# Performance work log

Hardware: AMD Instinct MI355X
Metric: run time of the kernel (lower is better)

## Reference

```python
import jax, jax.numpy as jnp
import numpy as np

NUM_HEADS = 16
DIM_HEADS = 64
DIM_INPUT = 1024
DIM = NUM_HEADS * DIM_HEADS  # 1024


def setup_inputs() -> dict:
    key = jax.random.key(0)
    ks = jax.random.split(key, 8)
    B, S = 2, 2048
    inputs = jax.random.normal(ks[0], (B, S, DIM_INPUT), dtype=jnp.float32)
    attention_mask = jnp.zeros((B, 1, 1, S), dtype=jnp.float32)
    s = 1.0 / np.sqrt(DIM_INPUT)
    Wq = jax.random.normal(ks[1], (DIM_INPUT, DIM), dtype=jnp.float32) * s
    bq = jnp.zeros((DIM,), dtype=jnp.float32)
    Wk = jax.random.normal(ks[2], (DIM_INPUT, DIM), dtype=jnp.float32) * s
    bk = jnp.zeros((DIM,), dtype=jnp.float32)
    Wv = jax.random.normal(ks[3], (DIM_INPUT, DIM), dtype=jnp.float32) * s
    bv = jnp.zeros((DIM,), dtype=jnp.float32)
    return {"inputs": inputs, "attention_mask": attention_mask,
            "Wq": Wq, "bq": bq, "Wk": Wk, "bk": bk, "Wv": Wv, "bv": bv}


def _split_heads(x):
    # [B, S, H*dh] -> [B, H, S, dh]
    B, S, _ = x.shape
    return x.reshape(B, S, NUM_HEADS, DIM_HEADS).transpose(0, 2, 1, 3)


def reference(inputs, attention_mask, Wq, bq, Wk, bk, Wv, bv):
    q = _split_heads(inputs @ Wq + bq)  # [B,H,S,dh]
    k = _split_heads(inputs @ Wk + bk)
    v = _split_heads(inputs @ Wv + bv)
    scores = jnp.einsum('bhsd,bhtd->bhst', q, k) / np.sqrt(DIM_HEADS).astype(np.float32)
    scores = scores + attention_mask  # broadcast additive mask
    probs = jax.nn.softmax(scores, axis=-1)  # dropout is identity in eval
    ctx = jnp.einsum('bhst,bhtd->bhsd', probs, v)  # [B,H,S,dh]
    B, H, S, dh = ctx.shape
    return ctx.transpose(0, 2, 1, 3).reshape(B, S, H * dh)
```

## Files before the change

### kernel.cpp

```cpp
#include <hip/hip_runtime.h>


typedef __attribute__((ext_vector_type(4))) float f32x4;
typedef __attribute__((ext_vector_type(16))) float f32x16;
typedef __attribute__((ext_vector_type(8))) __bf16 bf16x8;

#define DEV static __device__ __forceinline__

constexpr int S_ = 2048;
constexpr int H_ = 16;
constexpr int DH_ = 64;
constexpr int DIN_ = 1024;
constexpr int M_ = 2 * S_;
constexpr int N3_ = 3 * 1024;
constexpr int K_ = DIN_;
constexpr float LOG2E = 1.44269504088896340736f;

DEV unsigned short f2bf(float f) {
  unsigned u = __builtin_bit_cast(unsigned, f);
  u += 0x7fffu + ((u >> 16) & 1u);
  return (unsigned short)(u >> 16);
}

DEV unsigned cvt_pk(float lo, float hi) {
  unsigned d;
  asm("v_cvt_pk_bf16_f32 %0, %1, %2" : "=v"(d) : "v"(lo), "v"(hi));
  return d;
}

DEV void gload_lds16(const void* g, void* l) {
  __builtin_amdgcn_global_load_lds(
      (const __attribute__((address_space(1))) unsigned int*)g,
      (__attribute__((address_space(3))) unsigned int*)l, 16, 0, 0);
}

DEV int kswz(int row, int colb) { return row * 128 + (colb ^ ((row & 7) << 4)); }

__global__ __launch_bounds__(256) void convert_x(const float* __restrict__ X,
                                                 unsigned short* __restrict__ Xbf) {
  int idx = (blockIdx.x * 256 + threadIdx.x) * 8;
  float4 a = *(const float4*)(X + idx);
  float4 b = *(const float4*)(X + idx + 4);
  unsigned short r[8];
  r[0] = f2bf(a.x); r[1] = f2bf(a.y); r[2] = f2bf(a.z); r[3] = f2bf(a.w);
  r[4] = f2bf(b.x); r[5] = f2bf(b.y); r[6] = f2bf(b.z); r[7] = f2bf(b.w);
  *(uint4*)(Xbf + idx) = *(uint4*)r;
}

__global__ __launch_bounds__(256) void transpose_w(const float* __restrict__ Wq,
                                                   const float* __restrict__ Wk,
                                                   const float* __restrict__ Wv,
                                                   unsigned short* __restrict__ Wt) {
  __shared__ float tile[32][33];
  int z = blockIdx.z;
  const float* W = (z == 0) ? Wq : (z == 1) ? Wk : Wv;
  int n0 = blockIdx.x * 32, k0 = blockIdx.y * 32;
  int tx = threadIdx.x, ty = threadIdx.y;
  for (int i = 0; i < 4; ++i)
    tile[ty + i * 8][tx] = W[(size_t)(k0 + ty + i * 8) * 1024 + n0 + tx];
  __syncthreads();
  for (int i = 0; i < 4; ++i)
    Wt[(size_t)(z * 1024 + n0 + ty + i * 8) * 1024 + k0 + tx] =
        f2bf(tile[tx][ty + i * 8]);
}

__global__ __launch_bounds__(256, 2) void qkv_gemm(
    const unsigned short* __restrict__ Xbf, const unsigned short* __restrict__ Wt,
    const float* __restrict__ bq, const float* __restrict__ bk,
    const float* __restrict__ bv, unsigned short* __restrict__ Qw,
    unsigned short* __restrict__ Kw, unsigned short* __restrict__ Vt) {
  __shared__ unsigned short Abuf[128 * 64];
  __shared__ unsigned short Bbuf[128 * 64];
  int tid = threadIdx.x;
  int w = tid >> 6, l = tid & 63;
  int row16 = l & 15, kg = l >> 4;
  int mBase = blockIdx.y * 128, nBase = blockIdx.x * 128;
  int wm = w >> 1, wn = w & 1;

  f32x4 acc[4][4] = {};

  const int grow = l >> 3;
  const int gcol = ((l & 7) ^ grow) * 8;

  for (int kt = 0; kt < K_ / 64; ++kt) {
    int k0 = kt * 64;
    __syncthreads();
#pragma unroll
    for (int j = 0; j < 4; ++j) {
      int c1k = w * 4 + j;
      int r = c1k * 8 + grow;
      gload_lds16(Xbf + (size_t)(mBase + r) * K_ + k0 + gcol,
                  (char*)Abuf + c1k * 1024);
      gload_lds16(Wt + (size_t)(nBase + r) * K_ + k0 + gcol,
                  (char*)Bbuf + c1k * 1024);
    }
    __syncthreads();
#pragma unroll
    for (int kk = 0; kk < 2; ++kk) {
      bf16x8 af[4], bfr[4];
#pragma unroll
      for (int m = 0; m < 4; ++m)
        af[m] = *(const bf16x8*)((const char*)Abuf +
                 kswz(wm * 64 + m * 16 + row16, kk * 64 + kg * 16));
#pragma unroll
      for (int n = 0; n < 4; ++n)
        bfr[n] = *(const bf16x8*)((const char*)Bbuf +
                  kswz(wn * 64 + n * 16 + row16, kk * 64 + kg * 16));
#pragma unroll
      for (int m = 0; m < 4; ++m)
#pragma unroll
        for (int n = 0; n < 4; ++n)
          acc[m][n] = __builtin_amdgcn_mfma_f32_16x16x32_bf16(af[m], bfr[n],
                                                              acc[m][n], 0, 0, 0);
    }
  }

#pragma unroll
  for (int n = 0; n < 4; ++n) {
    int gn = nBase + wn * 64 + n * 16 + row16;
    int which = gn >> 10;
    int nn = gn & 1023;
    float bias = (which == 0 ? bq : which == 1 ? bk : bv)[nn];
    unsigned short* dst = (which == 0) ? Qw : (which == 1) ? Kw : Vt;
    float scl = (which == 0) ? 0.125f * LOG2E : 1.0f;
    int hh = nn >> 6, dd = nn & 63;
#pragma unroll
    for (int m = 0; m < 4; ++m) {
      int gm0 = mBase + wm * 64 + m * 16 + kg * 4;
#pragma unroll
      for (int j = 0; j < 4; ++j) {
        int gm = gm0 + j;
        int bb = gm >> 11, ss = gm & 2047;
        float v = (acc[m][n][j] + bias) * scl;
        size_t idx;
        if (which == 2) {
          int cs = (ss & ~63) | ((ss & 63) ^ ((dd & 7) << 3));
          idx = ((size_t)(bb * H_ + hh) * DH_ + dd) * S_ + cs;
        } else if (which == 1) {
          idx = ((size_t)(bb * H_ + hh) * S_ + ss) * DH_ + (dd ^ ((ss & 7) << 3));
        } else {
          idx = ((size_t)(bb * H_ + hh) * S_ + ss) * DH_ + dd;
        }
        dst[idx] = f2bf(v);
      }
    }
  }
}

__global__ __launch_bounds__(256, 2) void attn_fwd(
    const unsigned short* __restrict__ Qw, const unsigned short* __restrict__ Kw,
    const unsigned short* __restrict__ Vt, const float* __restrict__ mask,
    float* __restrict__ out) {
  __shared__ __align__(16) char LDS[73728];

  const int tid = threadIdx.x;
  const int w = tid >> 6, l = tid & 63;
  const int qg = w >> 1, thalf = w & 1;
  const int lq = l & 31, h = l >> 5;
  const int wgid = blockIdx.x;
  const int xcd = wgid & 7, ixd = wgid >> 3;
  const int bh = xcd + 8 * (ixd >> 4);
  const int qt = ixd & 15;
  const int b = bh >> 4, hh = bh & 15;
  const int q0 = qt * 128 + qg * 64;

  const char* KbB = (const char*)(Kw + (size_t)bh * S_ * DH_);
  const char* VbB = (const char*)(Vt + (size_t)bh * DH_ * S_);

  {
    const float* mrow = mask + (size_t)b * S_ + tid * 8;
    float4 m0 = *(const float4*)mrow;
    float4 m1 = *(const float4*)(mrow + 4);
    m0.x *= LOG2E; m0.y *= LOG2E; m0.z *= LOG2E; m0.w *= LOG2E;
    m1.x *= LOG2E; m1.y *= LOG2E; m1.z *= LOG2E; m1.w *= LOG2E;
    *(float4*)(LDS + tid * 32) = m0;
    *(float4*)(LDS + tid * 32 + 16) = m1;
  }

  bf16x8 qfA[4], qfB[4];
  {
    const unsigned short* qa = Qw + ((size_t)bh * S_ + q0 + lq) * DH_;
    const unsigned short* qb = qa + 32 * DH_;
#pragma unroll
    for (int kk = 0; kk < 4; ++kk) {
      qfA[kk] = *(const bf16x8*)(qa + kk * 16 + h * 8);
      qfB[kk] = *(const bf16x8*)(qb + kk * 16 + h * 8);
    }
  }

  int rb[4];
#pragma unroll
  for (int kk = 0; kk < 4; ++kk)
    rb[kk] = 8192 + thalf * 8192 + lq * 128 +
             ((kk * 32 + h * 16) ^ ((lq & 7) << 4));

  int voff[4];
#pragma unroll
  for (int i = 0; i < 4; ++i) {
    int Lb = (w * 4 + i) * 1024 + l * 16;
    voff[i] = ((Lb >> 7) & 63) * (S_ * 2) + (Lb >> 13) * 128 + (Lb & 127);
  }

  auto stage = [&](int pair, int buf) __attribute__((always_inline)) {
#pragma unroll
    for (int i = 0; i < 4; ++i) {
      const int c = w * 4 + i;
      gload_lds16(KbB + (size_t)pair * 16384 + c * 1024 + l * 16,
                  LDS + 8192 + buf * 16384 + c * 1024);
      gload_lds16(VbB + (size_t)pair * 256 + voff[i],
                  LDS + 40960 + buf * 16384 + c * 1024);
    }
  };

  stage(0, 0);
  __syncthreads();

  float lA = 0.f, lB = 0.f;
  f32x16 OA0 = {}, OA1 = {}, OB0 = {}, OB1 = {};

  auto body = [&](int p, int cur) __attribute__((always_inline)) {
    if (p < 15) stage(p + 1, cur ^ 1);

    const int mo = thalf * 256 + h * 16 + p * 512;
    f32x16 pA0, pA1, pB0, pB1;
#pragma unroll
    for (int r2 = 0; r2 < 4; ++r2) {
      f32x4 a = *(const f32x4*)(LDS + mo + r2 * 32);
      f32x4 b4 = *(const f32x4*)(LDS + mo + 128 + r2 * 32);
#pragma unroll
      for (int c = 0; c < 4; ++c) {
        pA0[4 * r2 + c] = a[c];  pB0[4 * r2 + c] = a[c];
        pA1[4 * r2 + c] = b4[c]; pB1[4 * r2 + c] = b4[c];
      }
    }

    __builtin_amdgcn_s_setprio(1);
#pragma unroll
    for (int kk = 0; kk < 4; ++kk) {
      bf16x8 kf0 = *(const bf16x8*)(LDS + rb[kk] + cur * 16384);
      bf16x8 kf1 = *(const bf16x8*)(LDS + rb[kk] + 4096 + cur * 16384);
      pA0 = __builtin_amdgcn_mfma_f32_32x32x16_bf16(kf0, qfA[kk], pA0, 0, 0, 0);
      pB0 = __builtin_amdgcn_mfma_f32_32x32x16_bf16(kf0, qfB[kk], pB0, 0, 0, 0);
      pA1 = __builtin_amdgcn_mfma_f32_32x32x16_bf16(kf1, qfA[kk], pA1, 0, 0, 0);
      pB1 = __builtin_amdgcn_mfma_f32_32x32x16_bf16(kf1, qfB[kk], pB1, 0, 0, 0);
    }
    __builtin_amdgcn_s_setprio(0);

#pragma unroll
    for (int i = 0; i < 16; ++i) {
      pA0[i] = __builtin_amdgcn_exp2f(pA0[i]);
      pA1[i] = __builtin_amdgcn_exp2f(pA1[i]);
      pB0[i] = __builtin_amdgcn_exp2f(pB0[i]);
      pB1[i] = __builtin_amdgcn_exp2f(pB1[i]);
    }

    {
      float sA[8], sB[8];
#pragma unroll
      for (int i = 0; i < 8; ++i) {
        sA[i] = (pA0[i] + pA0[i + 8]) + (pA1[i] + pA1[i + 8]);
        sB[i] = (pB0[i] + pB0[i + 8]) + (pB1[i] + pB1[i + 8]);
      }
      float rsA = ((sA[0] + sA[1]) + (sA[2] + sA[3])) +
                  ((sA[4] + sA[5]) + (sA[6] + sA[7]));
      float rsB = ((sB[0] + sB[1]) + (sB[2] + sB[3])) +
                  ((sB[4] + sB[5]) + (sB[6] + sB[7]));
      rsA += __shfl_xor(rsA, 32, 64);
      rsB += __shfl_xor(rsB, 32, 64);
      lA += rsA;
      lB += rsB;
    }

    unsigned wA0[8], wA1[8], wB0[8], wB1[8];
#pragma unroll
    for (int r2 = 0; r2 < 4; ++r2) {
      wA0[2 * r2]     = cvt_pk(pA0[4 * r2 + 0], pA0[4 * r2 + 1]);
      wA0[2 * r2 + 1] = cvt_pk(pA0[4 * r2 + 2], pA0[4 * r2 + 3]);
      wA1[2 * r2]     = cvt_pk(pA1[4 * r2 + 0], pA1[4 * r2 + 1]);
      wA1[2 * r2 + 1] = cvt_pk(pA1[4 * r2 + 2], pA1[4 * r2 + 3]);
      wB0[2 * r2]     = cvt_pk(pB0[4 * r2 + 0], pB0[4 * r2 + 1]);
      wB0[2 * r2 + 1] = cvt_pk(pB0[4 * r2 + 2], pB0[4 * r2 + 3]);
      wB1[2 * r2]     = cvt_pk(pB1[4 * r2 + 0], pB1[4 * r2 + 1]);
      wB1[2 * r2 + 1] = cvt_pk(pB1[4 * r2 + 2], pB1[4 * r2 + 3]);
    }

    __builtin_amdgcn_s_setprio(1);
#pragma unroll
    for (int s = 0; s < 4; ++s) {
      const unsigned* WA = (s < 2) ? wA0 : wA1;
      const unsigned* WB = (s < 2) ? wB0 : wB1;
      const int base = (s & 1) * 4;
      unsigned sA0 = h ? WA[base + 0] : WA[base + 2];
      unsigned sA1 = h ? WA[base + 1] : WA[base + 3];
      unsigned sB0 = h ? WB[base + 0] : WB[base + 2];
      unsigned sB1 = h ? WB[base + 1] : WB[base + 3];
      unsigned cA0 = (unsigned)__shfl_xor((int)sA0, 32, 64);
      unsigned cA1 = (unsigned)__shfl_xor((int)sA1, 32, 64);
      unsigned cB0 = (unsigned)__shfl_xor((int)sB0, 32, 64);
      unsigned cB1 = (unsigned)__shfl_xor((int)sB1, 32, 64);
      uint4 fA, fB;
      fA.x = h ? cA0 : WA[base + 0];
      fA.y = h ? cA1 : WA[base + 1];
      fA.z = h ? WA[base + 2] : cA0;
      fA.w = h ? WA[base + 3] : cA1;
      fB.x = h ? cB0 : WB[base + 0];
      fB.y = h ? cB1 : WB[base + 1];
      fB.z = h ? WB[base + 2] : cB0;
      fB.w = h ? WB[base + 3] : cB1;
      bf16x8 pfA = __builtin_bit_cast(bf16x8, fA);
      bf16x8 pfB = __builtin_bit_cast(bf16x8, fB);
      bf16x8 vf0 = *(const bf16x8*)(LDS + rb[s] + 32768 + cur * 16384);
      bf16x8 vf1 = *(const bf16x8*)(LDS + rb[s] + 36864 + cur * 16384);
      OA0 = __builtin_amdgcn_mfma_f32_32x32x16_bf16(vf0, pfA, OA0, 0, 0, 0);
      OB0 = __builtin_amdgcn_mfma_f32_32x32x16_bf16(vf0, pfB, OB0, 0, 0, 0);
      OA1 = __builtin_amdgcn_mfma_f32_32x32x16_bf16(vf1, pfA, OA1, 0, 0, 0);
      OB1 = __builtin_amdgcn_mfma_f32_32x32x16_bf16(vf1, pfB, OB1, 0, 0, 0);
    }
    __builtin_amdgcn_s_setprio(0);

    __syncthreads();
  };

#pragma unroll 1
  for (int pp = 0; pp < 8; ++pp) {
    body(2 * pp, 0);
    body(2 * pp + 1, 1);
  }

  char* Osc = LDS + 8192;
  float* Mp = (float*)LDS;
  const int sbase = (qg * 64 + l) * 256;
  const int sx = l & 15;
  if (thalf == 1) {
    const f32x16* Os[4] = {&OA0, &OA1, &OB0, &OB1};
#pragma unroll
    for (int r = 0; r < 4; ++r)
#pragma unroll
      for (int i = 0; i < 4; ++i) {
        f32x4 v;
#pragma unroll
        for (int c = 0; c < 4; ++c) v[c] = (*Os[r])[i * 4 + c];
        *(f32x4*)(Osc + sbase + (((r * 4 + i) ^ sx) << 4)) = v;
      }
    Mp[qg * 64 + l] = lA;
    Mp[128 + qg * 64 + l] = lB;
  }
  __syncthreads();
  if (thalf == 0) {
    f32x16* Os[4] = {&OA0, &OA1, &OB0, &OB1};
#pragma unroll
    for (int r = 0; r < 4; ++r)
#pragma unroll
      for (int i = 0; i < 4; ++i) {
        f32x4 v = *(const f32x4*)(Osc + sbase + (((r * 4 + i) ^ sx) << 4));
#pragma unroll
        for (int c = 0; c < 4; ++c) (*Os[r])[i * 4 + c] += v[c];
      }
    lA += Mp[qg * 64 + l];
    lB += Mp[128 + qg * 64 + l];

    float invA = 1.0f / lA, invB = 1.0f / lB;
    float* orA = out + ((size_t)b * S_ + q0 + lq) * 1024 + hh * 64;
    float* orB = out + ((size_t)b * S_ + q0 + 32 + lq) * 1024 + hh * 64;
#pragma unroll
    for (int r2 = 0; r2 < 4; ++r2) {
      f32x4 a0, a1, b0, b1;
#pragma unroll
      for (int c = 0; c < 4; ++c) {
        a0[c] = OA0[4 * r2 + c] * invA;
        a1[c] = OA1[4 * r2 + c] * invA;
        b0[c] = OB0[4 * r2 + c] * invB;
        b1[c] = OB1[4 * r2 + c] * invB;
      }
      *(f32x4*)&orA[r2 * 8 + h * 4] = a0;
      *(f32x4*)&orA[32 + r2 * 8 + h * 4] = a1;
      *(f32x4*)&orB[r2 * 8 + h * 4] = b0;
      *(f32x4*)&orB[32 + r2 * 8 + h * 4] = b1;
    }
  }
}

extern "C" void kernel_launch(void* const* d_in, const int* in_sizes, int n_in,
                              void* d_out, int out_size, void* d_ws, size_t ws_size,
                              hipStream_t stream) {
  const float* X = (const float*)d_in[0];
  const float* mask = (const float*)d_in[1];
  const float* Wq = (const float*)d_in[2];
  const float* bq = (const float*)d_in[3];
  const float* Wk = (const float*)d_in[4];
  const float* bk = (const float*)d_in[5];
  const float* Wv = (const float*)d_in[6];
  const float* bv = (const float*)d_in[7];
  float* out = (float*)d_out;

  char* ws = (char*)d_ws;
  unsigned short* Xbf = (unsigned short*)ws;
  unsigned short* Wt  = (unsigned short*)(ws + (size_t)(8 << 20));
  unsigned short* Qw  = (unsigned short*)(ws + (size_t)(14 << 20));
  unsigned short* Kw  = (unsigned short*)(ws + (size_t)(22 << 20));
  unsigned short* Vt  = (unsigned short*)(ws + (size_t)(30 << 20));

  convert_x<<<dim3(M_ * K_ / (256 * 8)), dim3(256), 0, stream>>>(X, Xbf);
  transpose_w<<<dim3(32, 32, 3), dim3(32, 8), 0, stream>>>(Wq, Wk, Wv, Wt);
  qkv_gemm<<<dim3(N3_ / 128, M_ / 128), dim3(256), 0, stream>>>(
      Xbf, Wt, bq, bk, bv, Qw, Kw, Vt);
  attn_fwd<<<dim3(512), dim3(256), 0, stream>>>(Qw, Kw, Vt, mask, out);
}
```

Measured before the change: 95.31 us.

## Split attention key tiles across four waves per query group and fuse prep kernels

The attention kernel goes from 256 to 512 threads per block. Each query group of 64 rows now has four waves, and each wave handles a quarter of every 128-key tile instead of a half. Q fragments and the mask are read from global memory inside the loop rather than held in registers or LDS, and the partial outputs are combined in two reduction stages through LDS. The V layout swizzle is widened to 128-column blocks to match the new LDS read pattern. The X conversion and weight-transpose kernels are merged into one launch to save a launch. The aim is more waves in flight and lower register pressure per wave, at the cost of extra global loads and a longer final reduction.

```diff
diff --git a/kernel.cpp b/kernel.cpp
--- a/kernel.cpp
+++ b/kernel.cpp
@@ -10,10 +10,9 @@
 constexpr int S_ = 2048;
 constexpr int H_ = 16;
 constexpr int DH_ = 64;
-constexpr int DIN_ = 1024;
 constexpr int M_ = 2 * S_;
 constexpr int N3_ = 3 * 1024;
-constexpr int K_ = DIN_;
+constexpr int K_ = 1024;
 constexpr float LOG2E = 1.44269504088896340736f;
 
 DEV unsigned short f2bf(float f) {
@@ -36,32 +35,33 @@
 
 DEV int kswz(int row, int colb) { return row * 128 + (colb ^ ((row & 7) << 4)); }
 
-__global__ __launch_bounds__(256) void convert_x(const float* __restrict__ X,
-                                                 unsigned short* __restrict__ Xbf) {
-  int idx = (blockIdx.x * 256 + threadIdx.x) * 8;
-  float4 a = *(const float4*)(X + idx);
-  float4 b = *(const float4*)(X + idx + 4);
-  unsigned short r[8];
-  r[0] = f2bf(a.x); r[1] = f2bf(a.y); r[2] = f2bf(a.z); r[3] = f2bf(a.w);
-  r[4] = f2bf(b.x); r[5] = f2bf(b.y); r[6] = f2bf(b.z); r[7] = f2bf(b.w);
-  *(uint4*)(Xbf + idx) = *(uint4*)r;
-}
-
-__global__ __launch_bounds__(256) void transpose_w(const float* __restrict__ Wq,
-                                                   const float* __restrict__ Wk,
-                                                   const float* __restrict__ Wv,
-                                                   unsigned short* __restrict__ Wt) {
+__global__ __launch_bounds__(256) void prep(
+    const float* __restrict__ X, const float* __restrict__ Wq,
+    const float* __restrict__ Wk, const float* __restrict__ Wv,
+    unsigned short* __restrict__ Xbf, unsigned short* __restrict__ Wt) {
   __shared__ float tile[32][33];
-  int z = blockIdx.z;
-  const float* W = (z == 0) ? Wq : (z == 1) ? Wk : Wv;
-  int n0 = blockIdx.x * 32, k0 = blockIdx.y * 32;
-  int tx = threadIdx.x, ty = threadIdx.y;
-  for (int i = 0; i < 4; ++i)
-    tile[ty + i * 8][tx] = W[(size_t)(k0 + ty + i * 8) * 1024 + n0 + tx];
-  __syncthreads();
-  for (int i = 0; i < 4; ++i)
-    Wt[(size_t)(z * 1024 + n0 + ty + i * 8) * 1024 + k0 + tx] =
-        f2bf(tile[tx][ty + i * 8]);
+  const int id = blockIdx.x;
+  const int tid = threadIdx.x;
+  if (id < 3072) {
+    int z = id >> 10, rem = id & 1023;
+    const float* W = (z == 0) ? Wq : (z == 1) ? Wk : Wv;
+    int n0 = (rem & 31) * 32, k0 = (rem >> 5) * 32;
+    int tx = tid & 31, ty = tid >> 5;
+    for (int i = 0; i < 4; ++i)
+      tile[ty + i * 8][tx] = W[(size_t)(k0 + ty + i * 8) * 1024 + n0 + tx];
+    __syncthreads();
+    for (int i = 0; i < 4; ++i)
+      Wt[(size_t)(z * 1024 + n0 + ty + i * 8) * 1024 + k0 + tx] =
+          f2bf(tile[tx][ty + i * 8]);
+  } else {
+    int idx = ((id - 3072) * 256 + tid) * 8;
+    float4 a = *(const float4*)(X + idx);
+    float4 b = *(const float4*)(X + idx + 4);
+    unsigned short r[8];
+    r[0] = f2bf(a.x); r[1] = f2bf(a.y); r[2] = f2bf(a.z); r[3] = f2bf(a.w);
+    r[4] = f2bf(b.x); r[5] = f2bf(b.y); r[6] = f2bf(b.z); r[7] = f2bf(b.w);
+    *(uint4*)(Xbf + idx) = *(uint4*)r;
+  }
 }
 
 __global__ __launch_bounds__(256, 2) void qkv_gemm(
@@ -134,7 +134,7 @@
         float v = (acc[m][n][j] + bias) * scl;
         size_t idx;
         if (which == 2) {
-          int cs = (ss & ~63) | ((ss & 63) ^ ((dd & 7) << 3));
+          int cs = (ss & ~127) | ((ss & 127) ^ ((dd & 15) << 3));
           idx = ((size_t)(bb * H_ + hh) * DH_ + dd) * S_ + cs;
         } else if (which == 1) {
           idx = ((size_t)(bb * H_ + hh) * S_ + ss) * DH_ + (dd ^ ((ss & 7) << 3));
@@ -147,68 +147,52 @@
   }
 }
 
-__global__ __launch_bounds__(256, 2) void attn_fwd(
+__global__ __launch_bounds__(512, 4) void attn_fwd(
     const unsigned short* __restrict__ Qw, const unsigned short* __restrict__ Kw,
     const unsigned short* __restrict__ Vt, const float* __restrict__ mask,
     float* __restrict__ out) {
-  __shared__ __align__(16) char LDS[73728];
+  __shared__ __align__(16) char LDS[69632];
 
   const int tid = threadIdx.x;
   const int w = tid >> 6, l = tid & 63;
-  const int qg = w >> 1, thalf = w & 1;
+  const int qg = w >> 2, tq = w & 3;
   const int lq = l & 31, h = l >> 5;
   const int wgid = blockIdx.x;
   const int xcd = wgid & 7, ixd = wgid >> 3;
   const int bh = xcd + 8 * (ixd >> 4);
   const int qt = ixd & 15;
   const int b = bh >> 4, hh = bh & 15;
-  const int q0 = qt * 128 + qg * 64;
-
-  const char* KbB = (const char*)(Kw + (size_t)bh * S_ * DH_);
-  const char* VbB = (const char*)(Vt + (size_t)bh * DH_ * S_);
-
-  {
-    const float* mrow = mask + (size_t)b * S_ + tid * 8;
-    float4 m0 = *(const float4*)mrow;
-    float4 m1 = *(const float4*)(mrow + 4);
-    m0.x *= LOG2E; m0.y *= LOG2E; m0.z *= LOG2E; m0.w *= LOG2E;
-    m1.x *= LOG2E; m1.y *= LOG2E; m1.z *= LOG2E; m1.w *= LOG2E;
-    *(float4*)(LDS + tid * 32) = m0;
-    *(float4*)(LDS + tid * 32 + 16) = m1;
-  }
-
-  bf16x8 qfA[4], qfB[4];
-  {
-    const unsigned short* qa = Qw + ((size_t)bh * S_ + q0 + lq) * DH_;
-    const unsigned short* qb = qa + 32 * DH_;
-#pragma unroll
-    for (int kk = 0; kk < 4; ++kk) {
-      qfA[kk] = *(const bf16x8*)(qa + kk * 16 + h * 8);
-      qfB[kk] = *(const bf16x8*)(qb + kk * 16 + h * 8);
-    }
-  }
-
-  int rb[4];
+  const int q0w = qt * 128 + qg * 64;
+
+  const char* Kb = (const char*)(Kw + (size_t)bh * S_ * DH_);
+  const char* Vb = (const char*)(Vt + (size_t)bh * DH_ * S_);
+  const unsigned short* qAp = Qw + ((size_t)bh * S_ + q0w + lq) * DH_;
+  const unsigned short* qBp = qAp + 32 * DH_;
+  const float* mp = mask + (size_t)b * S_;
+
+  int voff[2];
+#pragma unroll
+  for (int i = 0; i < 2; ++i) {
+    int Lb = (w * 2 + i) * 1024 + l * 16;
+    voff[i] = (Lb >> 8) * (S_ * 2) + (Lb & 255);
+  }
+
+  int rbK[4], rbV[2];
 #pragma unroll
   for (int kk = 0; kk < 4; ++kk)
-    rb[kk] = 8192 + thalf * 8192 + lq * 128 +
-             ((kk * 32 + h * 16) ^ ((lq & 7) << 4));
-
-  int voff[4];
-#pragma unroll
-  for (int i = 0; i < 4; ++i) {
-    int Lb = (w * 4 + i) * 1024 + l * 16;
-    voff[i] = ((Lb >> 7) & 63) * (S_ * 2) + (Lb >> 13) * 128 + (Lb & 127);
-  }
-
-  auto stage = [&](int pair, int buf) __attribute__((always_inline)) {
-#pragma unroll
-    for (int i = 0; i < 4; ++i) {
-      const int c = w * 4 + i;
-      gload_lds16(KbB + (size_t)pair * 16384 + c * 1024 + l * 16,
-                  LDS + 8192 + buf * 16384 + c * 1024);
-      gload_lds16(VbB + (size_t)pair * 256 + voff[i],
-                  LDS + 40960 + buf * 16384 + c * 1024);
+    rbK[kk] = 4096 + (tq * 32 + lq) * 128 + ((kk * 32 + h * 16) ^ ((lq & 7) << 4));
+#pragma unroll
+  for (int s = 0; s < 2; ++s)
+    rbV[s] = 20480 + lq * 256 + ((tq * 64 + s * 32 + h * 16) ^ ((lq & 15) << 4));
+
+  auto stage = [&](int p, int buf) __attribute__((always_inline)) {
+#pragma unroll
+    for (int i = 0; i < 2; ++i) {
+      const int c = w * 2 + i;
+      gload_lds16(Kb + (size_t)p * 16384 + c * 1024 + l * 16,
+                  LDS + 4096 + buf * 32768 + c * 1024);
+      gload_lds16(Vb + (size_t)p * 256 + voff[i],
+                  LDS + 20480 + buf * 32768 + c * 1024);
     }
   };
 
@@ -221,96 +205,77 @@
   auto body = [&](int p, int cur) __attribute__((always_inline)) {
     if (p < 15) stage(p + 1, cur ^ 1);
 
-    const int mo = thalf * 256 + h * 16 + p * 512;
-    f32x16 pA0, pA1, pB0, pB1;
+    f32x4 mk[4];
 #pragma unroll
     for (int r2 = 0; r2 < 4; ++r2) {
-      f32x4 a = *(const f32x4*)(LDS + mo + r2 * 32);
-      f32x4 b4 = *(const f32x4*)(LDS + mo + 128 + r2 * 32);
-#pragma unroll
-      for (int c = 0; c < 4; ++c) {
-        pA0[4 * r2 + c] = a[c];  pB0[4 * r2 + c] = a[c];
-        pA1[4 * r2 + c] = b4[c]; pB1[4 * r2 + c] = b4[c];
+      float4 m4 = *(const float4*)(mp + p * 128 + tq * 32 + 8 * r2 + 4 * h);
+      mk[r2][0] = m4.x * LOG2E; mk[r2][1] = m4.y * LOG2E;
+      mk[r2][2] = m4.z * LOG2E; mk[r2][3] = m4.w * LOG2E;
+    }
+
+    unsigned wA[8], wB[8];
+#pragma unroll
+    for (int g = 0; g < 2; ++g) {
+      const unsigned short* qp = g ? qAp : qBp;
+      f32x16 pq;
+#pragma unroll
+      for (int r2 = 0; r2 < 4; ++r2)
+#pragma unroll
+        for (int c = 0; c < 4; ++c) pq[4 * r2 + c] = mk[r2][c];
+
+      __builtin_amdgcn_s_setprio(1);
+#pragma unroll
+      for (int kk = 0; kk < 4; ++kk) {
+        bf16x8 qf = *(const bf16x8*)(qp + kk * 16 + h * 8);
+        bf16x8 kf = *(const bf16x8*)(LDS + rbK[kk] + cur * 32768);
+        pq = __builtin_amdgcn_mfma_f32_32x32x16_bf16(kf, qf, pq, 0, 0, 0);
+      }
+      __builtin_amdgcn_s_setprio(0);
+
+#pragma unroll
+      for (int i = 0; i < 16; ++i) pq[i] = __builtin_amdgcn_exp2f(pq[i]);
+
+      float s8[8];
+#pragma unroll
+      for (int i = 0; i < 8; ++i) s8[i] = pq[i] + pq[i + 8];
+      float rs = ((s8[0] + s8[1]) + (s8[2] + s8[3])) +
+                 ((s8[4] + s8[5]) + (s8[6] + s8[7]));
+      rs += __shfl_xor(rs, 32, 64);
+      if (g) lA += rs; else lB += rs;
+
+      unsigned* W = g ? wA : wB;
+#pragma unroll
+      for (int r2 = 0; r2 < 4; ++r2) {
+        W[2 * r2]     = cvt_pk(pq[4 * r2 + 0], pq[4 * r2 + 1]);
+        W[2 * r2 + 1] = cvt_pk(pq[4 * r2 + 2], pq[4 * r2 + 3]);
       }
     }
 
     __builtin_amdgcn_s_setprio(1);
 #pragma unroll
-    for (int kk = 0; kk < 4; ++kk) {
-      bf16x8 kf0 = *(const bf16x8*)(LDS + rb[kk] + cur * 16384);
-      bf16x8 kf1 = *(const bf16x8*)(LDS + rb[kk] + 4096 + cur * 16384);
-      pA0 = __builtin_amdgcn_mfma_f32_32x32x16_bf16(kf0, qfA[kk], pA0, 0, 0, 0);
-      pB0 = __builtin_amdgcn_mfma_f32_32x32x16_bf16(kf0, qfB[kk], pB0, 0, 0, 0);
-      pA1 = __builtin_amdgcn_mfma_f32_32x32x16_bf16(kf1, qfA[kk], pA1, 0, 0, 0);
-      pB1 = __builtin_amdgcn_mfma_f32_32x32x16_bf16(kf1, qfB[kk], pB1, 0, 0, 0);
-    }
-    __builtin_amdgcn_s_setprio(0);
-
-#pragma unroll
-    for (int i = 0; i < 16; ++i) {
-      pA0[i] = __builtin_amdgcn_exp2f(pA0[i]);
-      pA1[i] = __builtin_amdgcn_exp2f(pA1[i]);
-      pB0[i] = __builtin_amdgcn_exp2f(pB0[i]);
-      pB1[i] = __builtin_amdgcn_exp2f(pB1[i]);
-    }
-
-    {
-      float sA[8], sB[8];
-#pragma unroll
-      for (int i = 0; i < 8; ++i) {
-        sA[i] = (pA0[i] + pA0[i + 8]) + (pA1[i] + pA1[i + 8]);
-        sB[i] = (pB0[i] + pB0[i + 8]) + (pB1[i] + pB1[i + 8]);
-      }
-      float rsA = ((sA[0] + sA[1]) + (sA[2] + sA[3])) +
-                  ((sA[4] + sA[5]) + (sA[6] + sA[7]));
-      float rsB = ((sB[0] + sB[1]) + (sB[2] + sB[3])) +
-                  ((sB[4] + sB[5]) + (sB[6] + sB[7]));
-      rsA += __shfl_xor(rsA, 32, 64);
-      rsB += __shfl_xor(rsB, 32, 64);
-      lA += rsA;
-      lB += rsB;
-    }
-
-    unsigned wA0[8], wA1[8], wB0[8], wB1[8];
-#pragma unroll
-    for (int r2 = 0; r2 < 4; ++r2) {
-      wA0[2 * r2]     = cvt_pk(pA0[4 * r2 + 0], pA0[4 * r2 + 1]);
-      wA0[2 * r2 + 1] = cvt_pk(pA0[4 * r2 + 2], pA0[4 * r2 + 3]);
-      wA1[2 * r2]     = cvt_pk(pA1[4 * r2 + 0], pA1[4 * r2 + 1]);
-      wA1[2 * r2 + 1] = cvt_pk(pA1[4 * r2 + 2], pA1[4 * r2 + 3]);
-      wB0[2 * r2]     = cvt_pk(pB0[4 * r2 + 0], pB0[4 * r2 + 1]);
-      wB0[2 * r2 + 1] = cvt_pk(pB0[4 * r2 + 2], pB0[4 * r2 + 3]);
-      wB1[2 * r2]     = cvt_pk(pB1[4 * r2 + 0], pB1[4 * r2 + 1]);
-      wB1[2 * r2 + 1] = cvt_pk(pB1[4 * r2 + 2], pB1[4 * r2 + 3]);
-    }
-
-    __builtin_amdgcn_s_setprio(1);
-#pragma unroll
-    for (int s = 0; s < 4; ++s) {
-      const unsigned* WA = (s < 2) ? wA0 : wA1;
-      const unsigned* WB = (s < 2) ? wB0 : wB1;
-      const int base = (s & 1) * 4;
-      unsigned sA0 = h ? WA[base + 0] : WA[base + 2];
-      unsigned sA1 = h ? WA[base + 1] : WA[base + 3];
-      unsigned sB0 = h ? WB[base + 0] : WB[base + 2];
-      unsigned sB1 = h ? WB[base + 1] : WB[base + 3];
+    for (int s = 0; s < 2; ++s) {
+      const int base = s * 4;
+      unsigned sA0 = h ? wA[base + 0] : wA[base + 2];
+      unsigned sA1 = h ? wA[base + 1] : wA[base + 3];
+      unsigned sB0 = h ? wB[base + 0] : wB[base + 2];
+      unsigned sB1 = h ? wB[base + 1] : wB[base + 3];
       unsigned cA0 = (unsigned)__shfl_xor((int)sA0, 32, 64);
       unsigned cA1 = (unsigned)__shfl_xor((int)sA1, 32, 64);
       unsigned cB0 = (unsigned)__shfl_xor((int)sB0, 32, 64);
       unsigned cB1 = (unsigned)__shfl_xor((int)sB1, 32, 64);
       uint4 fA, fB;
-      fA.x = h ? cA0 : WA[base + 0];
-      fA.y = h ? cA1 : WA[base + 1];
-      fA.z = h ? WA[base + 2] : cA0;
-      fA.w = h ? WA[base + 3] : cA1;
-      fB.x = h ? cB0 : WB[base + 0];
-      fB.y = h ? cB1 : WB[base + 1];
-      fB.z = h ? WB[base + 2] : cB0;
-      fB.w = h ? WB[base + 3] : cB1;
+      fA.x = h ? cA0 : wA[base + 0];
+      fA.y = h ? cA1 : wA[base + 1];
+      fA.z = h ? wA[base + 2] : cA0;
+      fA.w = h ? wA[base + 3] : cA1;
+      fB.x = h ? cB0 : wB[base + 0];
+      fB.y = h ? cB1 : wB[base + 1];
+      fB.z = h ? wB[base + 2] : cB0;
+      fB.w = h ? wB[base + 3] : cB1;
       bf16x8 pfA = __builtin_bit_cast(bf16x8, fA);
       bf16x8 pfB = __builtin_bit_cast(bf16x8, fB);
-      bf16x8 vf0 = *(const bf16x8*)(LDS + rb[s] + 32768 + cur * 16384);
-      bf16x8 vf1 = *(const bf16x8*)(LDS + rb[s] + 36864 + cur * 16384);
+      bf16x8 vf0 = *(const bf16x8*)(LDS + rbV[s] + cur * 32768);
+      bf16x8 vf1 = *(const bf16x8*)(LDS + rbV[s] + 8192 + cur * 32768);
       OA0 = __builtin_amdgcn_mfma_f32_32x32x16_bf16(vf0, pfA, OA0, 0, 0, 0);
       OB0 = __builtin_amdgcn_mfma_f32_32x32x16_bf16(vf0, pfB, OB0, 0, 0, 0);
       OA1 = __builtin_amdgcn_mfma_f32_32x32x16_bf16(vf1, pfA, OA1, 0, 0, 0);
@@ -327,11 +292,15 @@
     body(2 * pp + 1, 1);
   }
 
-  char* Osc = LDS + 8192;
-  float* Mp = (float*)LDS;
-  const int sbase = (qg * 64 + l) * 256;
-  const int sx = l & 15;
-  if (thalf == 1) {
+  float* Lp = (float*)LDS;
+  char* SB = LDS + 4096;
+  const int lbase = ((qg * 4 + tq) * 64 + l) * 2;
+  Lp[lbase] = lA;
+  Lp[lbase + 1] = lB;
+
+  const int sx = (l & 15) << 4;
+  auto slotW = [&](int sid) __attribute__((always_inline)) {
+    char* sb = SB + sid * 16384 + l * 256;
     const f32x16* Os[4] = {&OA0, &OA1, &OB0, &OB1};
 #pragma unroll
     for (int r = 0; r < 4; ++r)
@@ -340,28 +309,39 @@
         f32x4 v;
 #pragma unroll
         for (int c = 0; c < 4; ++c) v[c] = (*Os[r])[i * 4 + c];
-        *(f32x4*)(Osc + sbase + (((r * 4 + i) ^ sx) << 4)) = v;
-      }
-    Mp[qg * 64 + l] = lA;
-    Mp[128 + qg * 64 + l] = lB;
-  }
+        *(f32x4*)(sb + (((r * 4 + i) * 16) ^ sx)) = v;
+      }
+  };
+  auto slotR = [&](int sid) __attribute__((always_inline)) {
+    char* sb = SB + sid * 16384 + l * 256;
+    f32x16* Os[4] = {&OA0, &OA1, &OB0, &OB1};
+#pragma unroll
+    for (int r = 0; r < 4; ++r)
+#pragma unroll
+      for (int i = 0; i < 4; ++i) {
+        f32x4 v = *(const f32x4*)(sb + (((r * 4 + i) * 16) ^ sx));
+#pragma unroll
+        for (int c = 0; c < 4; ++c) (*Os[r])[i * 4 + c] += v[c];
+      }
+  };
+
+  if (tq >= 2) slotW(qg * 2 + (tq - 2));
   __syncthreads();
-  if (thalf == 0) {
-    f32x16* Os[4] = {&OA0, &OA1, &OB0, &OB1};
-#pragma unroll
-    for (int r = 0; r < 4; ++r)
-#pragma unroll
-      for (int i = 0; i < 4; ++i) {
-        f32x4 v = *(const f32x4*)(Osc + sbase + (((r * 4 + i) ^ sx) << 4));
-#pragma unroll
-        for (int c = 0; c < 4; ++c) (*Os[r])[i * 4 + c] += v[c];
-      }
-    lA += Mp[qg * 64 + l];
-    lB += Mp[128 + qg * 64 + l];
-
-    float invA = 1.0f / lA, invB = 1.0f / lB;
-    float* orA = out + ((size_t)b * S_ + q0 + lq) * 1024 + hh * 64;
-    float* orB = out + ((size_t)b * S_ + q0 + 32 + lq) * 1024 + hh * 64;
+  if (tq < 2) slotR(qg * 2 + tq);
+  __syncthreads();
+  if (tq == 1) slotW(qg);
+  __syncthreads();
+  if (tq == 0) {
+    slotR(qg);
+    float sA = 0.f, sB = 0.f;
+#pragma unroll
+    for (int t = 0; t < 4; ++t) {
+      sA += Lp[((qg * 4 + t) * 64 + l) * 2];
+      sB += Lp[((qg * 4 + t) * 64 + l) * 2 + 1];
+    }
+    float invA = 1.0f / sA, invB = 1.0f / sB;
+    float* orA = out + ((size_t)b * S_ + q0w + lq) * 1024 + hh * 64;
+    float* orB = out + ((size_t)b * S_ + q0w + 32 + lq) * 1024 + hh * 64;
 #pragma unroll
     for (int r2 = 0; r2 < 4; ++r2) {
       f32x4 a0, a1, b0, b1;
@@ -400,9 +380,8 @@
   unsigned short* Kw  = (unsigned short*)(ws + (size_t)(22 << 20));
   unsigned short* Vt  = (unsigned short*)(ws + (size_t)(30 << 20));
 
-  convert_x<<<dim3(M_ * K_ / (256 * 8)), dim3(256), 0, stream>>>(X, Xbf);
-  transpose_w<<<dim3(32, 32, 3), dim3(32, 8), 0, stream>>>(Wq, Wk, Wv, Wt);
+  prep<<<dim3(3072 + 2048), dim3(256), 0, stream>>>(X, Wq, Wk, Wv, Xbf, Wt);
   qkv_gemm<<<dim3(N3_ / 128, M_ / 128), dim3(256), 0, stream>>>(
       Xbf, Wt, bq, bk, bv, Qw, Kw, Vt);
-  attn_fwd<<<dim3(512), dim3(256), 0, stream>>>(Qw, Kw, Vt, mask, out);
-}
+  attn_fwd<<<dim3(512), dim3(512), 0, stream>>>(Qw, Kw, Vt, mask, out);
+}
```

New measurement: 271.6 us. +185.0%, slower.
